# Kernel tuning notes

Measured on AMD Instinct MI355X. Metric: run time of the kernel, lower is better.

Reference implementation:

```python
import jax, jax.numpy as jnp
import numpy as np

# irreps kept in the output (sorted): 0e (dim 1), 1o (dim 3), 2e (dim 5)
IRS = (("0e", 1), ("1o", 3), ("2e", 5))
# multiplicity of each irrep in the reduced symmetric tensor product basis per order
MULS = {1: {"0e": 1, "1o": 1, "2e": 1},
        2: {"0e": 2, "1o": 2, "2e": 3},
        3: {"0e": 4, "1o": 6, "2e": 8}}
N, C, D, S, CORR = 1024, 128, 9, 10, 3  # nodes, channels, irreps dim (0e+1o+2e), species, correlation


def setup_inputs() -> dict:
    key = jax.random.key(0)
    ks = iter(jax.random.split(key, 64))
    inp = {"x": jax.random.normal(next(ks), (N, C, D), dtype=jnp.float32)}
    for order in range(1, CORR + 1):
        for ir, idim in IRS:
            mul = MULS[order][ir]
            # U basis tensor: shape (D,)*order + (mul, ir_dim); CG-like tensors are sparse
            u = jax.random.normal(next(ks), (D,) * order + (mul, idim), dtype=jnp.float32)
            mask = jax.random.bernoulli(next(ks), 0.25, u.shape)
            inp[f"u{order}_{ir}"] = jnp.where(mask, u, 0.0)
            # per-species weights, stddev mul**-0.5 ('element' gradient normalization)
            inp[f"w{order}_{ir}"] = jax.random.normal(next(ks), (S, mul, C), dtype=jnp.float32) * (mul ** -0.5)
    inp["index"] = jax.random.randint(next(ks), (N,), 0, S)
    return inp


def _forward(x, index, us, ws):
    # x: (N, C, D) node features; index: (N,) species ids
    out = {}
    for order in range(CORR, 0, -1):
        for ir, idim in IRS:
            w = ws[order][ir][index]  # per-species weight gather -> (N, mul, C)
            u = us[order][ir]          # (D,)*order + (mul, idim)
            if order == CORR:
                # highest order: contract one D axis with x together with the weights
                out[ir] = jnp.einsum('...jki,zkc,zcj->zc...i', u, w, x)
            else:
                # accumulate this order's term, then contract one more D axis with x
                acc = out[ir] + jnp.einsum('...ki,zkc->zc...i', u, w)
                out[ir] = jnp.einsum('zc...ji,zcj->zc...i', acc, x)
    # final out[ir]: (N, C, idim); axis_to_mul -> concat of (N, C*idim) blocks
    return jnp.concatenate([out[ir].reshape(N, C * idim) for ir, idim in IRS], axis=-1)


def reference(x, u1_0e, u1_1o, u1_2e, u2_0e, u2_1o, u2_2e, u3_0e, u3_1o, u3_2e,
              w1_0e, w1_1o, w1_2e, w2_0e, w2_1o, w2_2e, w3_0e, w3_1o, w3_2e, index):
    us = {1: {"0e": u1_0e, "1o": u1_1o, "2e": u1_2e},
          2: {"0e": u2_0e, "1o": u2_1o, "2e": u2_2e},
          3: {"0e": u3_0e, "1o": u3_1o, "2e": u3_2e}}
    ws = {1: {"0e": w1_0e, "1o": w1_1o, "2e": w1_2e},
          2: {"0e": w2_0e, "1o": w2_1o, "2e": w2_2e},
          3: {"0e": w3_0e, "1o": w3_1o, "2e": w3_2e}}
    return _forward(x, index, us, ws)
```

## Files before the change

### kernel.cpp

```cpp
#include <hip/hip_runtime.h>


#define NMONO 219
#define NN 1024
#define NC 128
#define NS 10
#define NPB 4
#define PADBLK 272
#define FOLD_CHUNK 16
#define NCHUNKF ((NMONO + FOLD_CHUNK - 1) / FOLD_CHUNK)

struct Tables { int mt[NMONO]; };

constexpr Tables make_tables() {
    Tables T{};
    int m = 0;
    for (int a = 0; a < 9; a++)
        for (int b = a; b < 10; b++)
            for (int j = b; j < 10; j++) { T.mt[m] = (a << 8) | (b << 4) | j; m++; }
    return T;
}
__device__ __constant__ const Tables TBL = make_tables();

__global__ __launch_bounds__(64) void u_sym(
    const float* __restrict__ u1_0e, const float* __restrict__ u1_1o, const float* __restrict__ u1_2e,
    const float* __restrict__ u2_0e, const float* __restrict__ u2_1o, const float* __restrict__ u2_2e,
    const float* __restrict__ u3_0e, const float* __restrict__ u3_1o, const float* __restrict__ u3_2e,
    float* __restrict__ usumAll)
{
    const int mono = blockIdx.x;
    const int t = threadIdx.x;
    const int e = TBL.mt[mono];
    const int A = (e >> 8) & 15, B = (e >> 4) & 15, J = e & 15;
    float sv = 0.f;
    if (J < 9) {
        if (t < 62) {
            const float* u; int mul, idim, k, i;
            if (t < 4)       { u = u3_0e; mul = 4; idim = 1; k = t; i = 0; }
            else if (t < 22) { u = u3_1o; mul = 6; idim = 3; int r = t - 4;  k = r / 3; i = r % 3; }
            else             { u = u3_2e; mul = 8; idim = 5; int r = t - 22; k = r / 5; i = r % 5; }
            int arr[6] = { A*81+B*9+J, A*81+J*9+B, B*81+A*9+J, B*81+J*9+A, J*81+A*9+B, J*81+B*9+A };
            for (int p = 0; p < 6; p++) {
                bool dup = false;
                for (int q = 0; q < p; q++) if (arr[q] == arr[p]) dup = true;
                if (!dup) sv += u[arr[p]*(mul*idim) + k*idim + i];
            }
        }
    } else if (B < 9) {
        if (t < 23) {
            const float* u; int mul, idim, k, i;
            if (t < 2)      { u = u2_0e; mul = 2; idim = 1; k = t; i = 0; }
            else if (t < 8) { u = u2_1o; mul = 2; idim = 3; int r = t - 2; k = r / 3; i = r % 3; }
            else            { u = u2_2e; mul = 3; idim = 5; int r = t - 8; k = r / 5; i = r % 5; }
            sv = u[(A*9+B)*(mul*idim) + k*idim + i];
            if (A != B) sv += u[(B*9+A)*(mul*idim) + k*idim + i];
        }
    } else {
        if (t < 9) {
            if (t == 0)      sv = u1_0e[A];
            else if (t < 4)  sv = u1_1o[A*3 + (t-1)];
            else             sv = u1_2e[A*5 + (t-4)];
        }
    }
    usumAll[mono*64 + t] = sv;
}

__global__ __launch_bounds__(128) void uw_fold(
    const float* __restrict__ w1_0e, const float* __restrict__ w1_1o, const float* __restrict__ w1_2e,
    const float* __restrict__ w2_0e, const float* __restrict__ w2_1o, const float* __restrict__ w2_2e,
    const float* __restrict__ w3_0e, const float* __restrict__ w3_1o, const float* __restrict__ w3_2e,
    const float* __restrict__ usumAll,
    float* __restrict__ uwA, float* __restrict__ uwB)
{
    const int s  = blockIdx.x / NCHUNKF;
    const int m0 = (blockIdx.x % NCHUNKF) * FOLD_CHUNK;
    const int c  = threadIdx.x;
    __shared__ float us[FOLD_CHUNK][64];

    for (int f = c; f < FOLD_CHUNK*64; f += 128) {
        const int mm = f >> 6, sl = f & 63, m = m0 + mm;
        us[mm][sl] = (m < NMONO) ? usumAll[m*64 + sl] : 0.f;
    }
    __syncthreads();

    float W30[4], W31[6], W32[8], W20[2], W21[2], W22[3];
    #pragma unroll
    for (int k = 0; k < 4; k++) W30[k] = w3_0e[(s*4+k)*NC + c];
    #pragma unroll
    for (int k = 0; k < 6; k++) W31[k] = w3_1o[(s*6+k)*NC + c];
    #pragma unroll
    for (int k = 0; k < 8; k++) W32[k] = w3_2e[(s*8+k)*NC + c];
    #pragma unroll
    for (int k = 0; k < 2; k++) W20[k] = w2_0e[(s*2+k)*NC + c];
    #pragma unroll
    for (int k = 0; k < 2; k++) W21[k] = w2_1o[(s*2+k)*NC + c];
    #pragma unroll
    for (int k = 0; k < 3; k++) W22[k] = w2_2e[(s*3+k)*NC + c];
    const float W10 = w1_0e[s*NC + c], W11 = w1_1o[s*NC + c], W12 = w1_2e[s*NC + c];

    for (int mm = 0; mm < FOLD_CHUNK; mm++) {
        const int m = m0 + mm;
        if (m >= NMONO) break;
        const int e = TBL.mt[m];
        const int B = (e >> 4) & 15, J = e & 15;
        float o[9];
        if (J < 9) {
            float v = 0.f;
            #pragma unroll
            for (int k = 0; k < 4; k++) v += us[mm][k] * W30[k];
            o[0] = v;
            #pragma unroll
            for (int i = 0; i < 3; i++) {
                v = 0.f;
                #pragma unroll
                for (int k = 0; k < 6; k++) v += us[mm][4 + k*3 + i] * W31[k];
                o[1+i] = v;
            }
            #pragma unroll
            for (int i = 0; i < 5; i++) {
                v = 0.f;
                #pragma unroll
                for (int k = 0; k < 8; k++) v += us[mm][22 + k*5 + i] * W32[k];
                o[4+i] = v;
            }
        } else if (B < 9) {
            float v = 0.f;
            #pragma unroll
            for (int k = 0; k < 2; k++) v += us[mm][k] * W20[k];
            o[0] = v;
            #pragma unroll
            for (int i = 0; i < 3; i++) {
                v = 0.f;
                #pragma unroll
                for (int k = 0; k < 2; k++) v += us[mm][2 + k*3 + i] * W21[k];
                o[1+i] = v;
            }
            #pragma unroll
            for (int i = 0; i < 5; i++) {
                v = 0.f;
                #pragma unroll
                for (int k = 0; k < 3; k++) v += us[mm][8 + k*5 + i] * W22[k];
                o[4+i] = v;
            }
        } else {
            o[0] = us[mm][0] * W10;
            #pragma unroll
            for (int i = 0; i < 3; i++) o[1+i] = us[mm][1+i] * W11;
            #pragma unroll
            for (int i = 0; i < 5; i++) o[4+i] = us[mm][4+i] * W12;
        }
        const size_t base = (size_t)(s*NMONO + m)*NC + c;
        float4 lo; lo.x = o[0]; lo.y = o[1]; lo.z = o[2]; lo.w = o[3];
        float4 hi; hi.x = o[4]; hi.y = o[5]; hi.z = o[6]; hi.w = o[7];
        *(float4*)(uwA + base*8)     = lo;
        *(float4*)(uwA + base*8 + 4) = hi;
        uwB[base] = o[8];
    }
}

__global__ __launch_bounds__(1024) void build_groups(
    const int* __restrict__ index,
    int* __restrict__ perm, int* __restrict__ offs, int* __restrict__ blockmap)
{
    __shared__ int cnt[NS], pos[NS], nbstart[NS+1];
    __shared__ int sh_nch;
    const int t = threadIdx.x;
    if (t < NS) cnt[t] = 0;
    __syncthreads();
    const int s = index[t];
    atomicAdd(&cnt[s], 1);
    __syncthreads();
    if (t == 0) {
        int o = 0, g = 0;
        for (int i = 0; i < NS; i++) {
            offs[i] = o; pos[i] = o; o += cnt[i];
            nbstart[i] = g; g += (cnt[i] + NPB - 1) / NPB;
        }
        offs[NS] = o; nbstart[NS] = g; sh_nch = g;
    }
    __syncthreads();
    const int Nch = sh_nch;
    for (int p = t; p < PADBLK; p += 1024) { blockmap[2*p] = -1; blockmap[2*p+1] = 0; }
    __syncthreads();
    if (t < Nch) {
        const int g = t;
        const int q = Nch >> 3, r = Nch & 7;
        int x = 0, stx = 0;
        for (int xx = 0; xx < 8; xx++) {
            const int cx = q + (xx < r ? 1 : 0);
            if (g < stx + cx) { x = xx; break; }
            stx += cx;
        }
        const int p = x + 8 * (g - stx);
        int sp = 0;
        while (g >= nbstart[sp+1]) sp++;
        blockmap[2*p]   = sp;
        blockmap[2*p+1] = g - nbstart[sp];
    }
    const int r2 = atomicAdd(&pos[s], 1);
    perm[r2] = t;
}

#define FMA_NODE(Q, P, F0, F1, FB)                                          \
    acc[Q][0] += F0.x*(P); acc[Q][1] += F0.y*(P); acc[Q][2] += F0.z*(P);    \
    acc[Q][3] += F0.w*(P); acc[Q][4] += F1.x*(P); acc[Q][5] += F1.y*(P);    \
    acc[Q][6] += F1.z*(P); acc[Q][7] += F1.w*(P); acc[Q][8] += FB*(P);

#define CONSUME(MM, F0, F1, FB)                                             \
    { const int e = TBL.mt[MM];                                             \
      const float4 xa = *(const float4*)&lx4[c44 + ((e>>8)&15)*4];          \
      const float4 xb = *(const float4*)&lx4[c44 + ((e>>4)&15)*4];          \
      const float4 xj = *(const float4*)&lx4[c44 + (e&15)*4];               \
      FMA_NODE(0, xa.x*xb.x*xj.x, F0, F1, FB)                               \
      FMA_NODE(1, xa.y*xb.y*xj.y, F0, F1, FB)                               \
      FMA_NODE(2, xa.z*xb.z*xj.z, F0, F1, FB)                               \
      FMA_NODE(3, xa.w*xb.w*xj.w, F0, F1, FB) }

__global__ __launch_bounds__(512, 4) void symcon_main(
    const float* __restrict__ x,
    const int* __restrict__ perm, const int* __restrict__ offs,
    const int* __restrict__ blockmap,
    const float* __restrict__ uwA, const float* __restrict__ uwB,
    float* __restrict__ out)
{
    __shared__ __align__(16) float lx4[128 * 44];
    __shared__ float red[2][128][36];

    const int tid = threadIdx.x;
    const int z   = tid >> 7;
    const int c   = tid & 127;
    const int c44 = c * 44;

    const int s     = blockmap[2*blockIdx.x];
    const int chunk = blockmap[2*blockIdx.x + 1];
    if (s < 0) return;
    const int gbeg = offs[s], gend = offs[s+1];
    const int p0   = gbeg + chunk*NPB;

    int node[4]; bool valid[4];
    #pragma unroll
    for (int q = 0; q < 4; q++) {
        const int pi = p0 + q;
        valid[q] = (pi < gend);
        node[q]  = perm[valid[q] ? pi : p0];
    }

    #pragma unroll
    for (int q = 0; q < 4; q++) {
        const size_t nb = (size_t)node[q] * 1152;
        for (int f = tid; f < 1152; f += 512) {
            const int ch = f / 9, d = f - ch*9;
            lx4[ch*44 + d*4 + q] = x[nb + f];
        }
    }
    { const int ch = tid >> 2, q = tid & 3; lx4[ch*44 + 36 + q] = 1.0f; }
    __syncthreads();

    float acc[4][9];
    #pragma unroll
    for (int q = 0; q < 4; q++)
        #pragma unroll
        for (int i = 0; i < 9; i++) acc[q][i] = 0.f;

    const int mbeg = 55 * z;
    const int mend = (z == 3) ? NMONO : 55 * (z + 1);

    const float* pa = uwA + ((size_t)(s*NMONO + mbeg)*NC + c) * 8;
    const float* pb = uwB +  (size_t)(s*NMONO + mbeg)*NC + c;

    float4 A0 = *(const float4*)pa, A1 = *(const float4*)(pa + 4); float Ab = *pb;
    float4 B0 = *(const float4*)(pa + NC*8), B1 = *(const float4*)(pa + NC*8 + 4); float Bb = *(pb + NC);

    for (int m = mbeg; m < mend; m += 2) {
        const bool h2 = (m + 2 < mend), h3 = (m + 3 < mend);
        const float* ra = h2 ? pa + 2*NC*8 : pa;
        const float* rb = h2 ? pb + 2*NC   : pb;
        const float* sa = h3 ? pa + 3*NC*8 : pa;
        const float* sb = h3 ? pb + 3*NC   : pb;
        const float4 nA0 = *(const float4*)ra, nA1 = *(const float4*)(ra + 4); const float nAb = *rb;
        const float4 nB0 = *(const float4*)sa, nB1 = *(const float4*)(sa + 4); const float nBb = *sb;
        CONSUME(m, A0, A1, Ab)
        if (m + 1 < mend) { CONSUME(m + 1, B0, B1, Bb) }
        A0 = nA0; A1 = nA1; Ab = nAb;
        B0 = nB0; B1 = nB1; Bb = nBb;
        pa += 2*NC*8; pb += 2*NC;
    }

    if (z >= 2) {
        float* r = &red[z-2][c][0];
        #pragma unroll
        for (int q = 0; q < 4; q++)
            #pragma unroll
            for (int i = 0; i < 9; i++) r[q*9 + i] = acc[q][i];
    }
    __syncthreads();
    if (z < 2) {
        const float* r = &red[z][c][0];
        #pragma unroll
        for (int q = 0; q < 4; q++)
            #pragma unroll
            for (int i = 0; i < 9; i++) acc[q][i] += r[q*9 + i];
    }
    __syncthreads();
    if (z == 1) {
        float* r = &red[0][c][0];
        #pragma unroll
        for (int q = 0; q < 4; q++)
            #pragma unroll
            for (int i = 0; i < 9; i++) r[q*9 + i] = acc[q][i];
    }
    __syncthreads();
    if (z == 0) {
        const float* r = &red[0][c][0];
        #pragma unroll
        for (int q = 0; q < 4; q++)
            #pragma unroll
            for (int i = 0; i < 9; i++) acc[q][i] += r[q*9 + i];
        #pragma unroll
        for (int q = 0; q < 4; q++) {
            if (!valid[q]) continue;
            float* orow = out + (size_t)node[q] * 1152;
            orow[c] = acc[q][0];
            #pragma unroll
            for (int i = 0; i < 3; i++) orow[128 + c*3 + i] = acc[q][1+i];
            #pragma unroll
            for (int i = 0; i < 5; i++) orow[512 + c*5 + i] = acc[q][4+i];
        }
    }
}

extern "C" void kernel_launch(void* const* d_in, const int* in_sizes, int n_in,
                              void* d_out, int out_size, void* d_ws, size_t ws_size,
                              hipStream_t stream)
{
    const float* x     = (const float*)d_in[0];
    const float* u1_0e = (const float*)d_in[1];
    const float* w1_0e = (const float*)d_in[2];
    const float* u1_1o = (const float*)d_in[3];
    const float* w1_1o = (const float*)d_in[4];
    const float* u1_2e = (const float*)d_in[5];
    const float* w1_2e = (const float*)d_in[6];
    const float* u2_0e = (const float*)d_in[7];
    const float* w2_0e = (const float*)d_in[8];
    const float* u2_1o = (const float*)d_in[9];
    const float* w2_1o = (const float*)d_in[10];
    const float* u2_2e = (const float*)d_in[11];
    const float* w2_2e = (const float*)d_in[12];
    const float* u3_0e = (const float*)d_in[13];
    const float* w3_0e = (const float*)d_in[14];
    const float* u3_1o = (const float*)d_in[15];
    const float* w3_1o = (const float*)d_in[16];
    const float* u3_2e = (const float*)d_in[17];
    const float* w3_2e = (const float*)d_in[18];
    const int*   index = (const int*)d_in[19];
    float* out = (float*)d_out;

    float* uwA     = (float*)d_ws;
    float* uwB     = uwA + (size_t)NS*NMONO*NC*8;
    float* usumAll = uwB + (size_t)NS*NMONO*NC;
    int*   perm     = (int*)(usumAll + NMONO*64);
    int*   offs     = perm + NN;
    int*   blockmap = offs + (NS+1);

    hipLaunchKernelGGL(build_groups, dim3(1), dim3(NN), 0, stream,
        index, perm, offs, blockmap);

    hipLaunchKernelGGL(u_sym, dim3(NMONO), dim3(64), 0, stream,
        u1_0e, u1_1o, u1_2e, u2_0e, u2_1o, u2_2e, u3_0e, u3_1o, u3_2e, usumAll);

    hipLaunchKernelGGL(uw_fold, dim3(NS*NCHUNKF), dim3(128), 0, stream,
        w1_0e, w1_1o, w1_2e, w2_0e, w2_1o, w2_2e, w3_0e, w3_1o, w3_2e,
        usumAll, uwA, uwB);

    hipLaunchKernelGGL(symcon_main, dim3(PADBLK), dim3(512), 0, stream,
        x, perm, offs, blockmap, uwA, uwB, out);
}
```

Measured before the change: 149.5 us.

## Merge prep kernels into one launch and split monomials across eight wave groups

The three setup kernels (grouping by species, U symmetrisation, U·W folding) become one prep kernel. Block 0 builds the permutation and block map, and the other blocks compute the symmetrised U slots inline instead of reading them from a workspace buffer. This removes two launches and the intermediate buffer round trip. The main kernel doubles its block size to 1024 threads, so the 219 monomials are split across 8 slices instead of 4, with a longer staged shared-memory reduction. That adds more synchronisation and register pressure under __launch_bounds__(1024,4).

```diff
diff --git a/kernel.cpp b/kernel.cpp
--- a/kernel.cpp
+++ b/kernel.cpp
@@ -22,15 +22,13 @@
 }
 __device__ __constant__ const Tables TBL = make_tables();
 
-__global__ __launch_bounds__(64) void u_sym(
+__device__ __forceinline__ float usum_slot(
+    int m, int t,
     const float* __restrict__ u1_0e, const float* __restrict__ u1_1o, const float* __restrict__ u1_2e,
     const float* __restrict__ u2_0e, const float* __restrict__ u2_1o, const float* __restrict__ u2_2e,
-    const float* __restrict__ u3_0e, const float* __restrict__ u3_1o, const float* __restrict__ u3_2e,
-    float* __restrict__ usumAll)
+    const float* __restrict__ u3_0e, const float* __restrict__ u3_1o, const float* __restrict__ u3_2e)
 {
-    const int mono = blockIdx.x;
-    const int t = threadIdx.x;
-    const int e = TBL.mt[mono];
+    const int e = TBL.mt[m];
     const int A = (e >> 8) & 15, B = (e >> 4) & 15, J = e & 15;
     float sv = 0.f;
     if (J < 9) {
@@ -62,27 +60,80 @@
             else             sv = u1_2e[A*5 + (t-4)];
         }
     }
-    usumAll[mono*64 + t] = sv;
-}
-
-__global__ __launch_bounds__(128) void uw_fold(
-    const float* __restrict__ w1_0e, const float* __restrict__ w1_1o, const float* __restrict__ w1_2e,
-    const float* __restrict__ w2_0e, const float* __restrict__ w2_1o, const float* __restrict__ w2_2e,
-    const float* __restrict__ w3_0e, const float* __restrict__ w3_1o, const float* __restrict__ w3_2e,
-    const float* __restrict__ usumAll,
-    float* __restrict__ uwA, float* __restrict__ uwB)
+    return sv;
+}
+
+__global__ __launch_bounds__(128) void prep(
+    const float* __restrict__ u1_0e, const float* __restrict__ w1_0e,
+    const float* __restrict__ u1_1o, const float* __restrict__ w1_1o,
+    const float* __restrict__ u1_2e, const float* __restrict__ w1_2e,
+    const float* __restrict__ u2_0e, const float* __restrict__ w2_0e,
+    const float* __restrict__ u2_1o, const float* __restrict__ w2_1o,
+    const float* __restrict__ u2_2e, const float* __restrict__ w2_2e,
+    const float* __restrict__ u3_0e, const float* __restrict__ w3_0e,
+    const float* __restrict__ u3_1o, const float* __restrict__ w3_1o,
+    const float* __restrict__ u3_2e, const float* __restrict__ w3_2e,
+    const int* __restrict__ index,
+    float* __restrict__ uwA, float* __restrict__ uwB,
+    int* __restrict__ perm, int* __restrict__ offs, int* __restrict__ blockmap)
 {
-    const int s  = blockIdx.x / NCHUNKF;
-    const int m0 = (blockIdx.x % NCHUNKF) * FOLD_CHUNK;
-    const int c  = threadIdx.x;
+    const int t = threadIdx.x;
+
+    if (blockIdx.x == 0) {
+        __shared__ int cnt[NS], pos[NS], nbstart[NS+1];
+        __shared__ int sh_nch;
+        if (t < NS) cnt[t] = 0;
+        __syncthreads();
+        for (int n = t; n < NN; n += 128) atomicAdd(&cnt[index[n]], 1);
+        __syncthreads();
+        if (t == 0) {
+            int o = 0, g = 0;
+            for (int i = 0; i < NS; i++) {
+                offs[i] = o; pos[i] = o; o += cnt[i];
+                nbstart[i] = g; g += (cnt[i] + NPB - 1) / NPB;
+            }
+            offs[NS] = o; nbstart[NS] = g; sh_nch = g;
+        }
+        __syncthreads();
+        const int Nch = sh_nch;
+        for (int p = t; p < PADBLK; p += 128) { blockmap[2*p] = -1; blockmap[2*p+1] = 0; }
+        __syncthreads();
+        for (int g = t; g < Nch; g += 128) {
+            const int q = Nch >> 3, r = Nch & 7;
+            int x = 0, stx = 0;
+            for (int xx = 0; xx < 8; xx++) {
+                const int cx = q + (xx < r ? 1 : 0);
+                if (g < stx + cx) { x = xx; break; }
+                stx += cx;
+            }
+            const int p = x + 8 * (g - stx);
+            int sp = 0;
+            while (g >= nbstart[sp+1]) sp++;
+            blockmap[2*p]   = sp;
+            blockmap[2*p+1] = g - nbstart[sp];
+        }
+        for (int n = t; n < NN; n += 128) {
+            const int s = index[n];
+            const int r = atomicAdd(&pos[s], 1);
+            perm[r] = n;
+        }
+        return;
+    }
+
+    const int b  = blockIdx.x - 1;
+    const int s  = b / NCHUNKF;
+    const int m0 = (b % NCHUNKF) * FOLD_CHUNK;
     __shared__ float us[FOLD_CHUNK][64];
 
-    for (int f = c; f < FOLD_CHUNK*64; f += 128) {
+    for (int f = t; f < FOLD_CHUNK*64; f += 128) {
         const int mm = f >> 6, sl = f & 63, m = m0 + mm;
-        us[mm][sl] = (m < NMONO) ? usumAll[m*64 + sl] : 0.f;
-    }
-    __syncthreads();
-
+        us[mm][sl] = (m < NMONO)
+            ? usum_slot(m, sl, u1_0e, u1_1o, u1_2e, u2_0e, u2_1o, u2_2e, u3_0e, u3_1o, u3_2e)
+            : 0.f;
+    }
+    __syncthreads();
+
+    const int c = t;
     float W30[4], W31[6], W32[8], W20[2], W21[2], W22[3];
     #pragma unroll
     for (int k = 0; k < 4; k++) W30[k] = w3_0e[(s*4+k)*NC + c];
@@ -156,49 +207,6 @@
         *(float4*)(uwA + base*8 + 4) = hi;
         uwB[base] = o[8];
     }
-}
-
-__global__ __launch_bounds__(1024) void build_groups(
-    const int* __restrict__ index,
-    int* __restrict__ perm, int* __restrict__ offs, int* __restrict__ blockmap)
-{
-    __shared__ int cnt[NS], pos[NS], nbstart[NS+1];
-    __shared__ int sh_nch;
-    const int t = threadIdx.x;
-    if (t < NS) cnt[t] = 0;
-    __syncthreads();
-    const int s = index[t];
-    atomicAdd(&cnt[s], 1);
-    __syncthreads();
-    if (t == 0) {
-        int o = 0, g = 0;
-        for (int i = 0; i < NS; i++) {
-            offs[i] = o; pos[i] = o; o += cnt[i];
-            nbstart[i] = g; g += (cnt[i] + NPB - 1) / NPB;
-        }
-        offs[NS] = o; nbstart[NS] = g; sh_nch = g;
-    }
-    __syncthreads();
-    const int Nch = sh_nch;
-    for (int p = t; p < PADBLK; p += 1024) { blockmap[2*p] = -1; blockmap[2*p+1] = 0; }
-    __syncthreads();
-    if (t < Nch) {
-        const int g = t;
-        const int q = Nch >> 3, r = Nch & 7;
-        int x = 0, stx = 0;
-        for (int xx = 0; xx < 8; xx++) {
-            const int cx = q + (xx < r ? 1 : 0);
-            if (g < stx + cx) { x = xx; break; }
-            stx += cx;
-        }
-        const int p = x + 8 * (g - stx);
-        int sp = 0;
-        while (g >= nbstart[sp+1]) sp++;
-        blockmap[2*p]   = sp;
-        blockmap[2*p+1] = g - nbstart[sp];
-    }
-    const int r2 = atomicAdd(&pos[s], 1);
-    perm[r2] = t;
 }
 
 #define FMA_NODE(Q, P, F0, F1, FB)                                          \
@@ -216,7 +224,21 @@
       FMA_NODE(2, xa.z*xb.z*xj.z, F0, F1, FB)                               \
       FMA_NODE(3, xa.w*xb.w*xj.w, F0, F1, FB) }
 
-__global__ __launch_bounds__(512, 4) void symcon_main(
+#define RED_WRITE(SLOT)                                                     \
+    { float* r = &red[SLOT][c][0];                                          \
+      _Pragma("unroll")                                                     \
+      for (int q = 0; q < 4; q++)                                           \
+          _Pragma("unroll")                                                 \
+          for (int i = 0; i < 9; i++) r[q*9 + i] = acc[q][i]; }
+
+#define RED_ADD(SLOT)                                                       \
+    { const float* r = &red[SLOT][c][0];                                    \
+      _Pragma("unroll")                                                     \
+      for (int q = 0; q < 4; q++)                                           \
+          _Pragma("unroll")                                                 \
+          for (int i = 0; i < 9; i++) acc[q][i] += r[q*9 + i]; }
+
+__global__ __launch_bounds__(1024, 4) void symcon_main(
     const float* __restrict__ x,
     const int* __restrict__ perm, const int* __restrict__ offs,
     const int* __restrict__ blockmap,
@@ -248,12 +270,12 @@
     #pragma unroll
     for (int q = 0; q < 4; q++) {
         const size_t nb = (size_t)node[q] * 1152;
-        for (int f = tid; f < 1152; f += 512) {
+        for (int f = tid; f < 1152; f += 1024) {
             const int ch = f / 9, d = f - ch*9;
             lx4[ch*44 + d*4 + q] = x[nb + f];
         }
     }
-    { const int ch = tid >> 2, q = tid & 3; lx4[ch*44 + 36 + q] = 1.0f; }
+    if (tid < 512) { const int ch = tid >> 2, q = tid & 3; lx4[ch*44 + 36 + q] = 1.0f; }
     __syncthreads();
 
     float acc[4][9];
@@ -262,8 +284,8 @@
         #pragma unroll
         for (int i = 0; i < 9; i++) acc[q][i] = 0.f;
 
-    const int mbeg = 55 * z;
-    const int mend = (z == 3) ? NMONO : 55 * (z + 1);
+    const int mbeg = (z < 3) ? 28*z : 84 + 27*(z - 3);
+    const int mend = mbeg + ((z < 3) ? 28 : 27);
 
     const float* pa = uwA + ((size_t)(s*NMONO + mbeg)*NC + c) * 8;
     const float* pb = uwB +  (size_t)(s*NMONO + mbeg)*NC + c;
@@ -286,36 +308,22 @@
         pa += 2*NC*8; pb += 2*NC;
     }
 
-    if (z >= 2) {
-        float* r = &red[z-2][c][0];
-        #pragma unroll
-        for (int q = 0; q < 4; q++)
-            #pragma unroll
-            for (int i = 0; i < 9; i++) r[q*9 + i] = acc[q][i];
-    }
-    __syncthreads();
-    if (z < 2) {
-        const float* r = &red[z][c][0];
-        #pragma unroll
-        for (int q = 0; q < 4; q++)
-            #pragma unroll
-            for (int i = 0; i < 9; i++) acc[q][i] += r[q*9 + i];
-    }
-    __syncthreads();
-    if (z == 1) {
-        float* r = &red[0][c][0];
-        #pragma unroll
-        for (int q = 0; q < 4; q++)
-            #pragma unroll
-            for (int i = 0; i < 9; i++) r[q*9 + i] = acc[q][i];
-    }
+    if (z == 2 || z == 3) RED_WRITE(z - 2)
+    __syncthreads();
+    if (z == 0 || z == 1) RED_ADD(z)
+    __syncthreads();
+    if (z == 6 || z == 7) RED_WRITE(z - 6)
+    __syncthreads();
+    if (z == 4 || z == 5) RED_ADD(z - 4)
+    __syncthreads();
+    if (z == 4 || z == 5) RED_WRITE(z - 4)
+    __syncthreads();
+    if (z == 0 || z == 1) RED_ADD(z)
+    __syncthreads();
+    if (z == 1) RED_WRITE(0)
     __syncthreads();
     if (z == 0) {
-        const float* r = &red[0][c][0];
-        #pragma unroll
-        for (int q = 0; q < 4; q++)
-            #pragma unroll
-            for (int i = 0; i < 9; i++) acc[q][i] += r[q*9 + i];
+        RED_ADD(0)
         #pragma unroll
         for (int q = 0; q < 4; q++) {
             if (!valid[q]) continue;
@@ -355,23 +363,18 @@
     const int*   index = (const int*)d_in[19];
     float* out = (float*)d_out;
 
-    float* uwA     = (float*)d_ws;
-    float* uwB     = uwA + (size_t)NS*NMONO*NC*8;
-    float* usumAll = uwB + (size_t)NS*NMONO*NC;
-    int*   perm     = (int*)(usumAll + NMONO*64);
+    float* uwA = (float*)d_ws;
+    float* uwB = uwA + (size_t)NS*NMONO*NC*8;
+    int*   perm     = (int*)(uwB + (size_t)NS*NMONO*NC);
     int*   offs     = perm + NN;
     int*   blockmap = offs + (NS+1);
 
-    hipLaunchKernelGGL(build_groups, dim3(1), dim3(NN), 0, stream,
-        index, perm, offs, blockmap);
-
-    hipLaunchKernelGGL(u_sym, dim3(NMONO), dim3(64), 0, stream,
-        u1_0e, u1_1o, u1_2e, u2_0e, u2_1o, u2_2e, u3_0e, u3_1o, u3_2e, usumAll);
-
-    hipLaunchKernelGGL(uw_fold, dim3(NS*NCHUNKF), dim3(128), 0, stream,
-        w1_0e, w1_1o, w1_2e, w2_0e, w2_1o, w2_2e, w3_0e, w3_1o, w3_2e,
-        usumAll, uwA, uwB);
-
-    hipLaunchKernelGGL(symcon_main, dim3(PADBLK), dim3(512), 0, stream,
+    hipLaunchKernelGGL(prep, dim3(1 + NS*NCHUNKF), dim3(128), 0, stream,
+        u1_0e, w1_0e, u1_1o, w1_1o, u1_2e, w1_2e,
+        u2_0e, w2_0e, u2_1o, w2_1o, u2_2e, w2_2e,
+        u3_0e, w3_0e, u3_1o, w3_1o, u3_2e, w3_2e,
+        index, uwA, uwB, perm, offs, blockmap);
+
+    hipLaunchKernelGGL(symcon_main, dim3(PADBLK), dim3(1024), 0, stream,
         x, perm, offs, blockmap, uwA, uwB, out);
 }
```

New measurement: 161.3 us. +7.9%, slower.
